# Performance work log

Measured on AMD Instinct MI355X. Metric: run time of the kernel, lower is better.

## Reference

```python
import jax, jax.numpy as jnp
import numpy as np

BN_EPS = 1e-5


def setup_inputs() -> dict:
    key = jax.random.key(0)
    k1, k2, k3 = jax.random.split(key, 3)
    B, C, R, N = 512, 256, 8, 81
    x = jax.random.normal(k1, (B, C, 9, 9), dtype=jnp.float32)
    adj = jax.random.uniform(k2, (B, R, N, N), dtype=jnp.float32)
    # xavier-uniform-like init for per-relation weights
    limit = float(np.sqrt(6.0 / (C + C)))
    weight = jax.random.uniform(k3, (R, C, C), dtype=jnp.float32, minval=-limit, maxval=limit)
    gamma = jnp.ones((C,), dtype=jnp.float32)
    beta = jnp.zeros((C,), dtype=jnp.float32)
    return {"x": x, "adj": adj, "weight": weight, "gamma": gamma, "beta": beta}


def reference(x, adj, weight, gamma, beta):
    B, C = x.shape[0], x.shape[1]
    N = 81
    # (B, C, 9, 9) -> (B, N, C) node features
    h = x.reshape(B, C, N).transpose(0, 2, 1)
    # per-relation message passing: msg_r = adj_r @ h, then msg_r @ W_r, summed over r
    msg = jnp.einsum('brnm,bmc->brnc', adj, h)          # (B, R, N, C)
    out_h = jnp.einsum('brnc,rcd->bnd', msg, weight)    # (B, N, C)
    out = out_h.transpose(0, 2, 1).reshape(B, C, 9, 9)
    pre = out + x
    # BatchNorm2d (training mode): biased batch stats over (N, H, W) per channel
    mean = jnp.mean(pre, axis=(0, 2, 3), keepdims=True)
    var = jnp.mean(jnp.square(pre - mean), axis=(0, 2, 3), keepdims=True)
    norm = (pre - mean) * jax.lax.rsqrt(var + BN_EPS)
    bn = norm * gamma[None, :, None, None] + beta[None, :, None, None]
    return jax.nn.relu(bn)
```

## Files before the change

kernel.cpp:

```cpp
#include <hip/hip_runtime.h>


#define B_SZ 512
#define C_SZ 256
#define R_SZ 8
#define N_SZ 81
#define TH 512

typedef short bf16x8 __attribute__((ext_vector_type(8)));
typedef float f32x4 __attribute__((ext_vector_type(4)));

__device__ __forceinline__ unsigned short f2bf(float f) {
    union { float f; unsigned u; } v; v.f = f;
    unsigned r = v.u + 0x7FFFu + ((v.u >> 16) & 1u);
    return (unsigned short)(r >> 16);
}

#define HT_OFF   0
#define ADJ_OFF  45056
#define MSG_OFF  53504
#define SMEM_SZ  (78080 + 32)

__device__ __forceinline__ int msg_addr(int row, int colbyte) {
    int s = (row ^ (row >> 3)) & 7;
    return MSG_OFF + row * 512 + (colbyte ^ (s << 4));
}

__global__ void prep_wt(const float* __restrict__ w, unsigned short* __restrict__ wt) {
    int i = blockIdx.x * blockDim.x + threadIdx.x;
    if (i >= R_SZ * C_SZ * C_SZ) return;
    int r = i >> 16;
    int d = (i >> 8) & 255;
    int c = i & 255;
    wt[i] = f2bf(w[(r * C_SZ + c) * C_SZ + d]);
}

__launch_bounds__(TH, 4)
__global__ void rgcn_main(const float* __restrict__ x,
                          const float* __restrict__ adj,
                          const unsigned short* __restrict__ wt,
                          float* __restrict__ out,
                          float* __restrict__ psum) {
    __shared__ __align__(16) unsigned char smem[SMEM_SZ];
    unsigned short* hT   = (unsigned short*)(smem + HT_OFF);
    unsigned short* adjs = (unsigned short*)(smem + ADJ_OFF);

    const int bid  = blockIdx.x;
    const int xcd  = bid & 7;
    const int slot = bid >> 3;
    const int b    = xcd * 64 + (slot >> 1);
    const int half = slot & 1;
    const int n0   = half * 48;

    const int tid  = threadIdx.x;
    const int lane = tid & 63;
    const int wave = tid >> 6;
    const int lr   = lane & 15;
    const int lk   = lane >> 4;

    const float* xb   = x + (size_t)b * C_SZ * N_SZ;
    const float* adjb = adj + ((size_t)b * R_SZ * N_SZ + n0) * N_SZ;
    const int cnt = half ? (33 * N_SZ) : (48 * N_SZ);

    float pf[8];
#pragma unroll
    for (int u = 0; u < 8; ++u) {
        int i2 = tid + u * TH;
        pf[u] = (i2 < cnt) ? adjb[i2] : 0.f;
    }

    for (int i = tid; i < 256 * 88; i += TH) {
        int c = i / 88, m = i - c * 88;
        hT[i] = (m < N_SZ) ? f2bf(xb[c * N_SZ + m]) : (unsigned short)0;
    }
    for (int i = tid; i < 48 * 88; i += TH) adjs[i] = 0;
    __syncthreads();
#pragma unroll
    for (int u = 0; u < 8; ++u) {
        int i2 = tid + u * TH;
        if (i2 < cnt) {
            int n = i2 / N_SZ, m = i2 - n * N_SZ;
            adjs[n * 88 + m] = f2bf(pf[u]);
        }
    }
    __syncthreads();

    const f32x4 vzero = {0.f, 0.f, 0.f, 0.f};
    const bf16x8 bz = {0, 0, 0, 0, 0, 0, 0, 0};
    f32x4 acc[3][2];
#pragma unroll
    for (int i = 0; i < 3; ++i)
#pragma unroll
        for (int j = 0; j < 2; ++j) acc[i][j] = vzero;

    const int colbase = wave * 32;

    for (int r = 0; r < R_SZ; ++r) {
        if (r < R_SZ - 1) {
            const float* an = adjb + (r + 1) * (N_SZ * N_SZ);
#pragma unroll
            for (int u = 0; u < 8; ++u) {
                int i2 = tid + u * TH;
                pf[u] = (i2 < cnt) ? an[i2] : 0.f;
            }
        }

        f32x4 macc[3][2];
#pragma unroll
        for (int i = 0; i < 3; ++i)
#pragma unroll
            for (int j = 0; j < 2; ++j) macc[i][j] = vzero;

#pragma unroll
        for (int kk = 0; kk < 3; ++kk) {
            const int kb = kk * 64 + lk * 16;
            bf16x8 afr[3], bfr[2];
#pragma unroll
            for (int i = 0; i < 3; ++i) {
                const unsigned char* p = (const unsigned char*)adjs + (i * 16 + lr) * 176 + kb;
                afr[i] = *(const bf16x8*)p;
            }
#pragma unroll
            for (int j = 0; j < 2; ++j) {
                const unsigned char* p = (const unsigned char*)hT + (colbase + j * 16 + lr) * 176 + kb;
                bfr[j] = *(const bf16x8*)p;
            }
            if (kk == 2 && lk == 3) {
#pragma unroll
                for (int i = 0; i < 3; ++i) afr[i] = bz;
#pragma unroll
                for (int j = 0; j < 2; ++j) bfr[j] = bz;
            }
#pragma unroll
            for (int i = 0; i < 3; ++i)
#pragma unroll
                for (int j = 0; j < 2; ++j)
                    macc[i][j] = __builtin_amdgcn_mfma_f32_16x16x32_bf16(afr[i], bfr[j], macc[i][j], 0, 0, 0);
        }
        __syncthreads();

#pragma unroll
        for (int i = 0; i < 3; ++i) {
            int rowb = i * 16 + lk * 4;
#pragma unroll
            for (int j = 0; j < 2; ++j) {
                int colb = (colbase + j * 16 + lr) * 2;
#pragma unroll
                for (int q = 0; q < 4; ++q)
                    *(unsigned short*)(smem + msg_addr(rowb + q, colb)) = f2bf(macc[i][j][q]);
            }
        }
        if (r < R_SZ - 1) {
#pragma unroll
            for (int u = 0; u < 8; ++u) {
                int i2 = tid + u * TH;
                if (i2 < cnt) {
                    int n = i2 / N_SZ, m = i2 - n * N_SZ;
                    adjs[n * 88 + m] = f2bf(pf[u]);
                }
            }
        }
        __syncthreads();

        const unsigned short* wr = wt + r * (C_SZ * C_SZ);
#pragma unroll
        for (int kk = 0; kk < 8; ++kk) {
            bf16x8 afr[3], bfr[2];
#pragma unroll
            for (int i = 0; i < 3; ++i)
                afr[i] = *(const bf16x8*)(smem + msg_addr(i * 16 + lr, kk * 64 + lk * 16));
#pragma unroll
            for (int j = 0; j < 2; ++j) {
                int d = colbase + j * 16 + lr;
                bfr[j] = *(const bf16x8*)&wr[d * 256 + kk * 32 + lk * 8];
            }
#pragma unroll
            for (int i = 0; i < 3; ++i)
#pragma unroll
                for (int j = 0; j < 2; ++j)
                    acc[i][j] = __builtin_amdgcn_mfma_f32_16x16x32_bf16(afr[i], bfr[j], acc[i][j], 0, 0, 0);
        }
    }

    float* outb = out + (size_t)b * C_SZ * N_SZ;
    float s1[2] = {0.f, 0.f}, s2[2] = {0.f, 0.f};
#pragma unroll
    for (int j = 0; j < 2; ++j) {
        int d = colbase + j * 16 + lr;
#pragma unroll
        for (int i = 0; i < 3; ++i) {
            int nb = n0 + i * 16 + lk * 4;
#pragma unroll
            for (int q = 0; q < 4; ++q) {
                int n = nb + q;
                if (n < N_SZ) {
                    float pre = acc[i][j][q] + xb[d * N_SZ + n];
                    outb[d * N_SZ + n] = pre;
                    s1[j] += pre;
                    s2[j] += pre * pre;
                }
            }
        }
    }
    const int bh = b * 2 + half;
#pragma unroll
    for (int j = 0; j < 2; ++j) {
        s1[j] += __shfl_down(s1[j], 32);  s1[j] += __shfl_down(s1[j], 16);
        s2[j] += __shfl_down(s2[j], 32);  s2[j] += __shfl_down(s2[j], 16);
    }
    if (lane < 16) {
#pragma unroll
        for (int j = 0; j < 2; ++j) {
            int d = colbase + j * 16 + lane;
            psum[(size_t)d * 1024 + bh] = s1[j];
            psum[(size_t)C_SZ * 1024 + (size_t)d * 1024 + bh] = s2[j];
        }
    }
}

__global__ void bn_stats(const float* __restrict__ psum,
                         const float* __restrict__ gamma, const float* __restrict__ beta,
                         float* __restrict__ mr) {
    int c = blockIdx.x;
    int t = threadIdx.x;
    float a = 0.f, s = 0.f;
    for (int k = t; k < 1024; k += 64) {
        a += psum[(size_t)c * 1024 + k];
        s += psum[(size_t)C_SZ * 1024 + (size_t)c * 1024 + k];
    }
#pragma unroll
    for (int off = 32; off > 0; off >>= 1) {
        a += __shfl_down(a, off);
        s += __shfl_down(s, off);
    }
    if (t == 0) {
        const float inv = 1.0f / (float)(B_SZ * N_SZ);
        float mean = a * inv;
        float var = s * inv - mean * mean;
        float rstd = rsqrtf(var + 1e-5f);
        float scale = rstd * gamma[c];
        mr[c] = scale;
        mr[256 + c] = beta[c] - mean * scale;
    }
}

__global__ void bn_apply(float* __restrict__ out, const float* __restrict__ mr) {
    const int total4 = (B_SZ * C_SZ * N_SZ) / 4;
    f32x4* o4 = (f32x4*)out;
    for (int i = blockIdx.x * blockDim.x + threadIdx.x; i < total4;
         i += gridDim.x * blockDim.x) {
        f32x4 v = o4[i];
        int e0 = i * 4;
#pragma unroll
        for (int k = 0; k < 4; ++k) {
            int c = ((e0 + k) / N_SZ) & 255;
            float t = v[k] * mr[c] + mr[256 + c];
            v[k] = t > 0.f ? t : 0.f;
        }
        o4[i] = v;
    }
}

extern "C" void kernel_launch(void* const* d_in, const int* in_sizes, int n_in,
                              void* d_out, int out_size, void* d_ws, size_t ws_size,
                              hipStream_t stream) {
    const float* x     = (const float*)d_in[0];
    const float* adj   = (const float*)d_in[1];
    const float* w     = (const float*)d_in[2];
    const float* gamma = (const float*)d_in[3];
    const float* beta  = (const float*)d_in[4];
    float* out = (float*)d_out;

    unsigned short* wt = (unsigned short*)d_ws;
    char* p = (char*)d_ws + (size_t)R_SZ * C_SZ * C_SZ * 2;
    float* psum = (float*)p;
    float* mr = (float*)(p + (size_t)2 * 1024 * C_SZ * 4);

    prep_wt<<<(R_SZ * C_SZ * C_SZ + 255) / 256, 256, 0, stream>>>(w, wt);
    rgcn_main<<<1024, TH, 0, stream>>>(x, adj, wt, out, psum);
    bn_stats<<<C_SZ, 64, 0, stream>>>(psum, gamma, beta, mr);
    bn_apply<<<2048, 256, 0, stream>>>(out, mr);
}
```

Measured before the change: 293.9 us.

## Keep node features in registers, transpose MFMA roles, prefetch weights

Each wave now loads its channel slice of the node features straight into MFMA register fragments, so the large transposed feature copy in shared memory goes away and LDS drops from about 78KB to about 33KB. Both GEMMs are transposed so that channels form the A operand and nodes the B operand. This lets the message tile be written to shared memory as packed 64-bit stores instead of scalar 16-bit stores. Weight fragments are double-buffered from global memory in chunks so their loads overlap the MFMAs, and the BN partial-sum reduction is reworked to match the new accumulator layout. The cost is more register pressure under launch bounds of 4 blocks per SM, and the feature loads from global are strided and uncoalesced.

```diff
diff --git a/kernel.cpp b/kernel.cpp
--- a/kernel.cpp
+++ b/kernel.cpp
@@ -16,14 +16,22 @@
     return (unsigned short)(r >> 16);
 }
 
-#define HT_OFF   0
-#define ADJ_OFF  45056
-#define MSG_OFF  53504
-#define SMEM_SZ  (78080 + 32)
-
-__device__ __forceinline__ int msg_addr(int row, int colbyte) {
-    int s = (row ^ (row >> 3)) & 7;
-    return MSG_OFF + row * 512 + (colbyte ^ (s << 4));
+__device__ __forceinline__ unsigned long long pack4bf(f32x4 v) {
+    unsigned long long r;
+    r  = (unsigned long long)f2bf(v[0]);
+    r |= (unsigned long long)f2bf(v[1]) << 16;
+    r |= (unsigned long long)f2bf(v[2]) << 32;
+    r |= (unsigned long long)f2bf(v[3]) << 48;
+    return r;
+}
+
+#define ADJ_OFF 0
+#define MSG_OFF 8448
+#define SMEM_SZ (8448 + 48 * 512 + 32)
+
+__device__ __forceinline__ int msg_addr(int n, int cbyte) {
+    int s = (n ^ (n >> 3)) & 7;
+    return MSG_OFF + n * 512 + (cbyte ^ (s << 4));
 }
 
 __global__ void prep_wt(const float* __restrict__ w, unsigned short* __restrict__ wt) {
@@ -42,7 +50,6 @@
                           float* __restrict__ out,
                           float* __restrict__ psum) {
     __shared__ __align__(16) unsigned char smem[SMEM_SZ];
-    unsigned short* hT   = (unsigned short*)(smem + HT_OFF);
     unsigned short* adjs = (unsigned short*)(smem + ADJ_OFF);
 
     const int bid  = blockIdx.x;
@@ -51,16 +58,35 @@
     const int b    = xcd * 64 + (slot >> 1);
     const int half = slot & 1;
     const int n0   = half * 48;
+    const int nvalid = half ? 33 : 48;
+    const int cnt  = nvalid * N_SZ;
 
     const int tid  = threadIdx.x;
     const int lane = tid & 63;
     const int wave = tid >> 6;
     const int lr   = lane & 15;
     const int lk   = lane >> 4;
+    const int cb   = wave * 32;
 
     const float* xb   = x + (size_t)b * C_SZ * N_SZ;
     const float* adjb = adj + ((size_t)b * R_SZ * N_SZ + n0) * N_SZ;
-    const int cnt = half ? (33 * N_SZ) : (48 * N_SZ);
+
+    bf16x8 hfr[3][2];
+#pragma unroll
+    for (int kk = 0; kk < 3; ++kk) {
+#pragma unroll
+        for (int jc = 0; jc < 2; ++jc) {
+            int c = cb + jc * 16 + lr;
+            const float* src = xb + c * N_SZ;
+#pragma unroll
+            for (int e = 0; e < 8; ++e) {
+                int m = kk * 32 + lk * 8 + e;
+                hfr[kk][jc][e] = (m < N_SZ) ? (short)f2bf(src[m]) : (short)0;
+            }
+        }
+    }
+
+    for (int i = tid; i < (48 * 88) / 2; i += TH) ((unsigned*)adjs)[i] = 0;
 
     float pf[8];
 #pragma unroll
@@ -68,12 +94,6 @@
         int i2 = tid + u * TH;
         pf[u] = (i2 < cnt) ? adjb[i2] : 0.f;
     }
-
-    for (int i = tid; i < 256 * 88; i += TH) {
-        int c = i / 88, m = i - c * 88;
-        hT[i] = (m < N_SZ) ? f2bf(xb[c * N_SZ + m]) : (unsigned short)0;
-    }
-    for (int i = tid; i < 48 * 88; i += TH) adjs[i] = 0;
     __syncthreads();
 #pragma unroll
     for (int u = 0; u < 8; ++u) {
@@ -86,14 +106,11 @@
     __syncthreads();
 
     const f32x4 vzero = {0.f, 0.f, 0.f, 0.f};
-    const bf16x8 bz = {0, 0, 0, 0, 0, 0, 0, 0};
-    f32x4 acc[3][2];
-#pragma unroll
-    for (int i = 0; i < 3; ++i)
-#pragma unroll
-        for (int j = 0; j < 2; ++j) acc[i][j] = vzero;
-
-    const int colbase = wave * 32;
+    f32x4 acc[2][3];
+#pragma unroll
+    for (int jd = 0; jd < 2; ++jd)
+#pragma unroll
+        for (int jn = 0; jn < 3; ++jn) acc[jd][jn] = vzero;
 
     for (int r = 0; r < R_SZ; ++r) {
         if (r < R_SZ - 1) {
@@ -105,49 +122,42 @@
             }
         }
 
-        f32x4 macc[3][2];
-#pragma unroll
-        for (int i = 0; i < 3; ++i)
-#pragma unroll
-            for (int j = 0; j < 2; ++j) macc[i][j] = vzero;
+        f32x4 macc[2][3];
+#pragma unroll
+        for (int jc = 0; jc < 2; ++jc)
+#pragma unroll
+            for (int jn = 0; jn < 3; ++jn) macc[jc][jn] = vzero;
 
 #pragma unroll
         for (int kk = 0; kk < 3; ++kk) {
-            const int kb = kk * 64 + lk * 16;
-            bf16x8 afr[3], bfr[2];
-#pragma unroll
-            for (int i = 0; i < 3; ++i) {
-                const unsigned char* p = (const unsigned char*)adjs + (i * 16 + lr) * 176 + kb;
-                afr[i] = *(const bf16x8*)p;
-            }
-#pragma unroll
-            for (int j = 0; j < 2; ++j) {
-                const unsigned char* p = (const unsigned char*)hT + (colbase + j * 16 + lr) * 176 + kb;
-                bfr[j] = *(const bf16x8*)p;
-            }
-            if (kk == 2 && lk == 3) {
-#pragma unroll
-                for (int i = 0; i < 3; ++i) afr[i] = bz;
-#pragma unroll
-                for (int j = 0; j < 2; ++j) bfr[j] = bz;
-            }
-#pragma unroll
-            for (int i = 0; i < 3; ++i)
-#pragma unroll
-                for (int j = 0; j < 2; ++j)
-                    macc[i][j] = __builtin_amdgcn_mfma_f32_16x16x32_bf16(afr[i], bfr[j], macc[i][j], 0, 0, 0);
-        }
+            bf16x8 bfr[3];
+#pragma unroll
+            for (int jn = 0; jn < 3; ++jn)
+                bfr[jn] = *(const bf16x8*)&adjs[(jn * 16 + lr) * 88 + kk * 32 + lk * 8];
+#pragma unroll
+            for (int jc = 0; jc < 2; ++jc)
+#pragma unroll
+                for (int jn = 0; jn < 3; ++jn)
+                    macc[jc][jn] = __builtin_amdgcn_mfma_f32_16x16x32_bf16(hfr[kk][jc], bfr[jn], macc[jc][jn], 0, 0, 0);
+        }
+
+        const unsigned short* wr = wt + r * (C_SZ * C_SZ);
+        bf16x8 wA[2][2], wB[2][2];
+#pragma unroll
+        for (int dk = 0; dk < 2; ++dk)
+#pragma unroll
+            for (int jd = 0; jd < 2; ++jd)
+                wA[dk][jd] = *(const bf16x8*)&wr[(cb + jd * 16 + lr) * 256 + dk * 32 + lk * 8];
+
         __syncthreads();
 
 #pragma unroll
-        for (int i = 0; i < 3; ++i) {
-            int rowb = i * 16 + lk * 4;
-#pragma unroll
-            for (int j = 0; j < 2; ++j) {
-                int colb = (colbase + j * 16 + lr) * 2;
-#pragma unroll
-                for (int q = 0; q < 4; ++q)
-                    *(unsigned short*)(smem + msg_addr(rowb + q, colb)) = f2bf(macc[i][j][q]);
+        for (int jc = 0; jc < 2; ++jc) {
+#pragma unroll
+            for (int jn = 0; jn < 3; ++jn) {
+                int n = jn * 16 + lr;
+                int cbyte = (cb + jc * 16 + lk * 4) * 2;
+                *(unsigned long long*)(smem + msg_addr(n, cbyte)) = pack4bf(macc[jc][jn]);
             }
         }
         if (r < R_SZ - 1) {
@@ -162,58 +172,71 @@
         }
         __syncthreads();
 
-        const unsigned short* wr = wt + r * (C_SZ * C_SZ);
-#pragma unroll
-        for (int kk = 0; kk < 8; ++kk) {
-            bf16x8 afr[3], bfr[2];
-#pragma unroll
-            for (int i = 0; i < 3; ++i)
-                afr[i] = *(const bf16x8*)(smem + msg_addr(i * 16 + lr, kk * 64 + lk * 16));
-#pragma unroll
-            for (int j = 0; j < 2; ++j) {
-                int d = colbase + j * 16 + lr;
-                bfr[j] = *(const bf16x8*)&wr[d * 256 + kk * 32 + lk * 8];
-            }
-#pragma unroll
-            for (int i = 0; i < 3; ++i)
-#pragma unroll
-                for (int j = 0; j < 2; ++j)
-                    acc[i][j] = __builtin_amdgcn_mfma_f32_16x16x32_bf16(afr[i], bfr[j], acc[i][j], 0, 0, 0);
-        }
+        auto do2 = [&](bf16x8 (&wc)[2][2], bf16x8 (&wn)[2][2], int kk0, bool load) {
+            if (load) {
+#pragma unroll
+                for (int dk = 0; dk < 2; ++dk)
+#pragma unroll
+                    for (int jd = 0; jd < 2; ++jd)
+                        wn[dk][jd] = *(const bf16x8*)&wr[(cb + jd * 16 + lr) * 256 + (kk0 + 2 + dk) * 32 + lk * 8];
+            }
+#pragma unroll
+            for (int dk = 0; dk < 2; ++dk) {
+                int kk = kk0 + dk;
+                bf16x8 bfr[3];
+#pragma unroll
+                for (int jn = 0; jn < 3; ++jn)
+                    bfr[jn] = *(const bf16x8*)(smem + msg_addr(jn * 16 + lr, kk * 64 + lk * 16));
+#pragma unroll
+                for (int jd = 0; jd < 2; ++jd)
+#pragma unroll
+                    for (int jn = 0; jn < 3; ++jn)
+                        acc[jd][jn] = __builtin_amdgcn_mfma_f32_16x16x32_bf16(wc[dk][jd], bfr[jn], acc[jd][jn], 0, 0, 0);
+            }
+        };
+        do2(wA, wB, 0, true);
+        do2(wB, wA, 2, true);
+        do2(wA, wB, 4, true);
+        do2(wB, wA, 6, false);
     }
 
     float* outb = out + (size_t)b * C_SZ * N_SZ;
-    float s1[2] = {0.f, 0.f}, s2[2] = {0.f, 0.f};
-#pragma unroll
-    for (int j = 0; j < 2; ++j) {
-        int d = colbase + j * 16 + lr;
-#pragma unroll
-        for (int i = 0; i < 3; ++i) {
-            int nb = n0 + i * 16 + lk * 4;
+    const int bh = b * 2 + half;
+#pragma unroll
+    for (int jd = 0; jd < 2; ++jd) {
+        float s1[4] = {0.f, 0.f, 0.f, 0.f};
+        float s2[4] = {0.f, 0.f, 0.f, 0.f};
+#pragma unroll
+        for (int jn = 0; jn < 3; ++jn) {
+            int nloc = jn * 16 + lr;
+            bool ok = nloc < nvalid;
+            int n = n0 + nloc;
 #pragma unroll
             for (int q = 0; q < 4; ++q) {
-                int n = nb + q;
-                if (n < N_SZ) {
-                    float pre = acc[i][j][q] + xb[d * N_SZ + n];
+                int d = cb + jd * 16 + lk * 4 + q;
+                if (ok) {
+                    float pre = acc[jd][jn][q] + xb[d * N_SZ + n];
                     outb[d * N_SZ + n] = pre;
-                    s1[j] += pre;
-                    s2[j] += pre * pre;
+                    s1[q] += pre;
+                    s2[q] += pre * pre;
                 }
             }
         }
-    }
-    const int bh = b * 2 + half;
-#pragma unroll
-    for (int j = 0; j < 2; ++j) {
-        s1[j] += __shfl_down(s1[j], 32);  s1[j] += __shfl_down(s1[j], 16);
-        s2[j] += __shfl_down(s2[j], 32);  s2[j] += __shfl_down(s2[j], 16);
-    }
-    if (lane < 16) {
-#pragma unroll
-        for (int j = 0; j < 2; ++j) {
-            int d = colbase + j * 16 + lane;
-            psum[(size_t)d * 1024 + bh] = s1[j];
-            psum[(size_t)C_SZ * 1024 + (size_t)d * 1024 + bh] = s2[j];
+#pragma unroll
+        for (int q = 0; q < 4; ++q) {
+#pragma unroll
+            for (int msk = 8; msk > 0; msk >>= 1) {
+                s1[q] += __shfl_xor(s1[q], msk);
+                s2[q] += __shfl_xor(s2[q], msk);
+            }
+        }
+        if (lr == 0) {
+#pragma unroll
+            for (int q = 0; q < 4; ++q) {
+                int d = cb + jd * 16 + lk * 4 + q;
+                psum[(size_t)d * 1024 + bh] = s1[q];
+                psum[(size_t)C_SZ * 1024 + (size_t)d * 1024 + bh] = s2[q];
+            }
         }
     }
 }
```

Result: faster. 235.5 us (-19.9%).
